# Kernel tuning notes

Measured on AMD Instinct MI355X. Metric: run time of the kernel, lower is better.

## Reference

```python
import jax, jax.numpy as jnp
import numpy as np

KS = 3          # ksize
PAD = 1         # (ksize-1)//2 * dilation, dilation=1

def setup_inputs() -> dict:
    key = jax.random.key(0)
    k1, k2, k3, k4 = jax.random.split(key, 4)
    B, NI, C, H, W = 4, 64, 64, 256, 256
    features = jax.random.normal(k1, (B, NI, H, W), jnp.float32)
    inpt = jax.random.normal(k2, (B, C, H, W), jnp.float32)
    # get_filter: Conv2d(ni, ksize**2, 3, padding=1 reflect, stride=1)
    w = jax.random.normal(k3, (KS * KS, NI, 3, 3), jnp.float32) * 0.05
    b = jax.random.normal(k4, (KS * KS,), jnp.float32) * 0.01
    return {"features": features, "inpt": inpt, "w": w, "b": b}

def reference(features, inpt, w, b):
    # 1) predict per-pixel filters: 3x3 conv with reflect padding
    fpad = jnp.pad(features, ((0, 0), (0, 0), (1, 1), (1, 1)), mode="reflect")
    ff = jax.lax.conv_general_dilated(
        fpad, w, window_strides=(1, 1), padding="VALID",
        dimension_numbers=("NCHW", "OIHW", "NCHW"),
    ) + b[None, :, None, None]                       # [B, 9, H, W]
    ff = jax.nn.softmax(ff, axis=1)                  # softmax over the 9 taps

    # 2) apply per-pixel filter to inpt (shared across channels)
    B, C, H, W = inpt.shape
    ipad = jnp.pad(inpt, ((0, 0), (0, 0), (PAD, PAD), (PAD, PAD)), mode="reflect")
    # unfold: taps in row-major (ki, kj) order, matching torch nn.Unfold
    patches = jnp.stack(
        [ipad[:, :, i:i + H, j:j + W] for i in range(KS) for j in range(KS)],
        axis=2,
    )                                                # [B, C, 9, H, W]
    # out[b,c,h,w] = sum_k patches[b,c,k,h,w] * ff[b,k,h,w]
    return jnp.einsum("bckhw,bkhw->bchw", patches, ff)
```

## Files before the change

kernel.cpp:

```cpp
#include <hip/hip_runtime.h>
#include <math.h>

#define BB 4
#define NI 64
#define CC 64
#define HH 256
#define WW 256
#define HW (HH * WW)

#define TW 64
#define TH 8
#define SR 10
#define SC 66
#define SE 660
#define BUFW 672
#define BUFSTRIDE 1344

__device__ __forceinline__ int refl(int i, int n) {
    i = (i < 0) ? -i : i;
    return (i >= n) ? (2 * n - 2 - i) : i;
}

__global__ __launch_bounds__(512) void pff_lds(
    const float* __restrict__ features,
    const float* __restrict__ inpt,
    const float* __restrict__ wgt,
    const float* __restrict__ bias,
    float* __restrict__ out)
{
    __shared__ float lds[4608];

    const int tid  = threadIdx.x;
    const int half = __builtin_amdgcn_readfirstlane(tid >> 8);
    const int p    = tid & 255;
    const int c    = p & 63;
    const int tr   = p >> 6;
    const int W0   = blockIdx.x * TW;
    const int H0   = blockIdx.y * TH;
    const int b    = blockIdx.z;

    int goff[3], loff[3];
    #pragma unroll
    for (int t = 0; t < 3; ++t) {
        int e = p + 256 * t;
        if (e >= SE) e -= 148;
        loff[t] = e;
        const int row = e / SC;
        const int col = e - row * SC;
        const int gh = refl(H0 - 1 + row, HH);
        const int gw = refl(W0 - 1 + col, WW);
        goff[t] = gh * WW + gw;
    }

    float accA[9], accB[9];
    #pragma unroll
    for (int k = 0; k < 9; ++k) { accA[k] = 0.f; accB[k] = 0.f; }

    const float* fb = features + (size_t)b * NI * HW + (size_t)half * 32 * HW;
    float r0 = fb[goff[0]], r1 = fb[goff[1]], r2 = fb[goff[2]];

    for (int ni = 0; ni < 32; ++ni) {
        float* bw = &lds[(ni & 1) * BUFSTRIDE + half * BUFW];
        bw[loff[0]] = r0; bw[loff[1]] = r1; bw[loff[2]] = r2;
        if (ni < 31) {
            const float* fn = fb + (size_t)(ni + 1) * HW;
            r0 = fn[goff[0]]; r1 = fn[goff[1]]; r2 = fn[goff[2]];
        }
        __syncthreads();

        float f[12];
        #pragma unroll
        for (int rr = 0; rr < 4; ++rr) {
            const float* br = bw + (2 * tr + rr) * SC + c;
            f[rr * 3 + 0] = br[0];
            f[rr * 3 + 1] = br[1];
            f[rr * 3 + 2] = br[2];
        }

        const float* wn = wgt + (half * 32 + ni) * 9;
        #pragma unroll
        for (int k = 0; k < 9; ++k) {
            const float* wk = wn + k * (NI * 9);
            const float w0 = wk[0], w1 = wk[1], w2 = wk[2];
            const float w3 = wk[3], w4 = wk[4], w5 = wk[5];
            const float w6 = wk[6], w7 = wk[7], w8 = wk[8];
            accA[k] = fmaf(f[0],  w0, accA[k]);
            accB[k] = fmaf(f[3],  w0, accB[k]);
            accA[k] = fmaf(f[1],  w1, accA[k]);
            accB[k] = fmaf(f[4],  w1, accB[k]);
            accA[k] = fmaf(f[2],  w2, accA[k]);
            accB[k] = fmaf(f[5],  w2, accB[k]);
            accA[k] = fmaf(f[3],  w3, accA[k]);
            accB[k] = fmaf(f[6],  w3, accB[k]);
            accA[k] = fmaf(f[4],  w4, accA[k]);
            accB[k] = fmaf(f[7],  w4, accB[k]);
            accA[k] = fmaf(f[5],  w5, accA[k]);
            accB[k] = fmaf(f[8],  w5, accB[k]);
            accA[k] = fmaf(f[6],  w6, accA[k]);
            accB[k] = fmaf(f[9],  w6, accB[k]);
            accA[k] = fmaf(f[7],  w7, accA[k]);
            accB[k] = fmaf(f[10], w7, accB[k]);
            accA[k] = fmaf(f[8],  w8, accA[k]);
            accB[k] = fmaf(f[11], w8, accB[k]);
        }
    }

    __syncthreads();
    #pragma unroll
    for (int k = 0; k < 9; ++k) lds[half * 2304 + k * 256 + p] = accA[k];
    __syncthreads();
    #pragma unroll
    for (int k = 0; k < 9; ++k)
        accA[k] = lds[k * 256 + p] + lds[2304 + k * 256 + p] + bias[k];
    __syncthreads();
    #pragma unroll
    for (int k = 0; k < 9; ++k) lds[half * 2304 + k * 256 + p] = accB[k];
    __syncthreads();
    #pragma unroll
    for (int k = 0; k < 9; ++k)
        accB[k] = lds[k * 256 + p] + lds[2304 + k * 256 + p] + bias[k];

    {
        float m = accA[0];
        #pragma unroll
        for (int k = 1; k < 9; ++k) m = fmaxf(m, accA[k]);
        float s = 0.f;
        #pragma unroll
        for (int k = 0; k < 9; ++k) { accA[k] = __expf(accA[k] - m); s += accA[k]; }
        const float inv = 1.f / s;
        #pragma unroll
        for (int k = 0; k < 9; ++k) accA[k] *= inv;
    }
    {
        float m = accB[0];
        #pragma unroll
        for (int k = 1; k < 9; ++k) m = fmaxf(m, accB[k]);
        float s = 0.f;
        #pragma unroll
        for (int k = 0; k < 9; ++k) { accB[k] = __expf(accB[k] - m); s += accB[k]; }
        const float inv = 1.f / s;
        #pragma unroll
        for (int k = 0; k < 9; ++k) accB[k] *= inv;
    }

    const float* ib = inpt + (size_t)b * CC * HW + (size_t)half * 32 * HW;
    float* ob       = out  + (size_t)b * CC * HW + (size_t)half * 32 * HW;
    const int oA = (H0 + 2 * tr) * WW + W0 + c;
    const int oB = oA + WW;

    r0 = ib[goff[0]]; r1 = ib[goff[1]]; r2 = ib[goff[2]];
    __syncthreads();

    for (int ch = 0; ch < 32; ++ch) {
        float* bw = &lds[(ch & 1) * BUFSTRIDE + half * BUFW];
        bw[loff[0]] = r0; bw[loff[1]] = r1; bw[loff[2]] = r2;
        if (ch < 31) {
            const float* in2 = ib + (size_t)(ch + 1) * HW;
            r0 = in2[goff[0]]; r1 = in2[goff[1]]; r2 = in2[goff[2]];
        }
        __syncthreads();

        float f[12];
        #pragma unroll
        for (int rr = 0; rr < 4; ++rr) {
            const float* br = bw + (2 * tr + rr) * SC + c;
            f[rr * 3 + 0] = br[0];
            f[rr * 3 + 1] = br[1];
            f[rr * 3 + 2] = br[2];
        }

        float vA = accA[0] * f[0];
        float vB = accB[0] * f[3];
        vA = fmaf(accA[1], f[1],  vA);  vB = fmaf(accB[1], f[4],  vB);
        vA = fmaf(accA[2], f[2],  vA);  vB = fmaf(accB[2], f[5],  vB);
        vA = fmaf(accA[3], f[3],  vA);  vB = fmaf(accB[3], f[6],  vB);
        vA = fmaf(accA[4], f[4],  vA);  vB = fmaf(accB[4], f[7],  vB);
        vA = fmaf(accA[5], f[5],  vA);  vB = fmaf(accB[5], f[8],  vB);
        vA = fmaf(accA[6], f[6],  vA);  vB = fmaf(accB[6], f[9],  vB);
        vA = fmaf(accA[7], f[7],  vA);  vB = fmaf(accB[7], f[10], vB);
        vA = fmaf(accA[8], f[8],  vA);  vB = fmaf(accB[8], f[11], vB);
        ob[(size_t)ch * HW + oA] = vA;
        ob[(size_t)ch * HW + oB] = vB;
    }
}

extern "C" void kernel_launch(void* const* d_in, const int* in_sizes, int n_in,
                              void* d_out, int out_size, void* d_ws, size_t ws_size,
                              hipStream_t stream) {
    const float* features = (const float*)d_in[0];
    const float* inpt     = (const float*)d_in[1];
    const float* wgt      = (const float*)d_in[2];
    const float* bias     = (const float*)d_in[3];
    float* out            = (float*)d_out;

    dim3 grid(WW / TW, HH / TH, BB);
    dim3 block(512);
    pff_lds<<<grid, block, 0, stream>>>(features, inpt, wgt, bias, out);
}
```

Before: 74.34 us.

## Give each wavefront a private LDS staging tile to drop block barriers

Each of the eight wavefronts now stages its own 4x66 halo tile in a private double-buffered LDS region. This removes the per-iteration __syncthreads in both the conv loop and the apply loop, relying on wave-synchronous execution instead. The cost is redundant global loads of overlapping halo rows, about twice the staged data, and more LDS use. The first inpt slice load is also hoisted above the cross-half reduction so it overlaps with that step.

New measurement: 70.30 us. 5.4% less time.

```diff
diff --git a/kernel.cpp b/kernel.cpp
--- a/kernel.cpp
+++ b/kernel.cpp
@@ -8,70 +8,69 @@
 #define WW 256
 #define HW (HH * WW)
 
-#define TW 64
-#define TH 8
-#define SR 10
-#define SC 66
-#define SE 660
-#define BUFW 672
-#define BUFSTRIDE 1344
+#define SRW 68
+#define BUFW 272
+#define NBUF 2
 
 __device__ __forceinline__ int refl(int i, int n) {
     i = (i < 0) ? -i : i;
     return (i >= n) ? (2 * n - 2 - i) : i;
 }
 
-__global__ __launch_bounds__(512) void pff_lds(
+__global__ __launch_bounds__(512) void pff_wave(
     const float* __restrict__ features,
     const float* __restrict__ inpt,
     const float* __restrict__ wgt,
     const float* __restrict__ bias,
     float* __restrict__ out)
 {
-    __shared__ float lds[4608];
+    __shared__ float stage[8][NBUF * BUFW];
+    __shared__ float part[2][9][256];
 
     const int tid  = threadIdx.x;
-    const int half = __builtin_amdgcn_readfirstlane(tid >> 8);
+    const int wv   = __builtin_amdgcn_readfirstlane(tid >> 6);
+    const int half = wv >> 2;
+    const int tr   = wv & 3;
+    const int l    = tid & 63;
     const int p    = tid & 255;
-    const int c    = p & 63;
-    const int tr   = p >> 6;
-    const int W0   = blockIdx.x * TW;
-    const int H0   = blockIdx.y * TH;
-    const int b    = blockIdx.z;
+    const int W0 = blockIdx.x * 64;
+    const int H0 = blockIdx.y * 8;
+    const int b  = blockIdx.z;
 
-    int goff[3], loff[3];
+    int goff[5], loff[5];
     #pragma unroll
-    for (int t = 0; t < 3; ++t) {
-        int e = p + 256 * t;
-        if (e >= SE) e -= 148;
-        loff[t] = e;
-        const int row = e / SC;
-        const int col = e - row * SC;
-        const int gh = refl(H0 - 1 + row, HH);
-        const int gw = refl(W0 - 1 + col, WW);
-        goff[t] = gh * WW + gw;
+    for (int t = 0; t < 5; ++t) {
+        const int e = (t < 4) ? (l + 64 * t) : (256 + (l & 7));
+        const int row = e / 66, col = e - row * 66;
+        loff[t] = row * SRW + col;
+        goff[t] = refl(H0 + 2 * tr - 1 + row, HH) * WW + refl(W0 - 1 + col, WW);
     }
+    const bool do5 = (l < 8);
 
     float accA[9], accB[9];
     #pragma unroll
     for (int k = 0; k < 9; ++k) { accA[k] = 0.f; accB[k] = 0.f; }
 
+    float* sb = &stage[wv][0];
+
     const float* fb = features + (size_t)b * NI * HW + (size_t)half * 32 * HW;
-    float r0 = fb[goff[0]], r1 = fb[goff[1]], r2 = fb[goff[2]];
+    float r0 = fb[goff[0]], r1 = fb[goff[1]], r2 = fb[goff[2]], r3 = fb[goff[3]];
+    float r4 = do5 ? fb[goff[4]] : 0.f;
 
     for (int ni = 0; ni < 32; ++ni) {
-        float* bw = &lds[(ni & 1) * BUFSTRIDE + half * BUFW];
-        bw[loff[0]] = r0; bw[loff[1]] = r1; bw[loff[2]] = r2;
+        float* bw = sb + (ni & 1) * BUFW;
+        bw[loff[0]] = r0; bw[loff[1]] = r1; bw[loff[2]] = r2; bw[loff[3]] = r3;
+        if (do5) bw[loff[4]] = r4;
         if (ni < 31) {
             const float* fn = fb + (size_t)(ni + 1) * HW;
-            r0 = fn[goff[0]]; r1 = fn[goff[1]]; r2 = fn[goff[2]];
+            r0 = fn[goff[0]]; r1 = fn[goff[1]]; r2 = fn[goff[2]]; r3 = fn[goff[3]];
+            if (do5) r4 = fn[goff[4]];
         }
-        __syncthreads();
 
         float f[12];
         #pragma unroll
         for (int rr = 0; rr < 4; ++rr) {
-            const float* br = bw + (2 * tr + rr) * SC + c;
+            const float* br = bw + rr * SRW + l;
             f[rr * 3 + 0] = br[0];
             f[rr * 3 + 1] = br[1];
             f[rr * 3 + 2] = br[2];
@@ -105,20 +104,21 @@
         }
     }
 
+    const float* ib = inpt + (size_t)b * CC * HW + (size_t)half * 32 * HW;
+    r0 = ib[goff[0]]; r1 = ib[goff[1]]; r2 = ib[goff[2]]; r3 = ib[goff[3]];
+    if (do5) r4 = ib[goff[4]];
+
+    #pragma unroll
+    for (int k = 0; k < 9; ++k) part[half][k][p] = accA[k];
     __syncthreads();
     #pragma unroll
-    for (int k = 0; k < 9; ++k) lds[half * 2304 + k * 256 + p] = accA[k];
+    for (int k = 0; k < 9; ++k) accA[k] = part[0][k][p] + part[1][k][p] + bias[k];
     __syncthreads();
     #pragma unroll
-    for (int k = 0; k < 9; ++k)
-        accA[k] = lds[k * 256 + p] + lds[2304 + k * 256 + p] + bias[k];
+    for (int k = 0; k < 9; ++k) part[half][k][p] = accB[k];
     __syncthreads();
     #pragma unroll
-    for (int k = 0; k < 9; ++k) lds[half * 2304 + k * 256 + p] = accB[k];
-    __syncthreads();
-    #pragma unroll
-    for (int k = 0; k < 9; ++k)
-        accB[k] = lds[k * 256 + p] + lds[2304 + k * 256 + p] + bias[k];
+    for (int k = 0; k < 9; ++k) accB[k] = part[0][k][p] + part[1][k][p] + bias[k];
 
     {
         float m = accA[0];
@@ -143,27 +143,24 @@
         for (int k = 0; k < 9; ++k) accB[k] *= inv;
     }
 
-    const float* ib = inpt + (size_t)b * CC * HW + (size_t)half * 32 * HW;
-    float* ob       = out  + (size_t)b * CC * HW + (size_t)half * 32 * HW;
-    const int oA = (H0 + 2 * tr) * WW + W0 + c;
+    float* ob = out + (size_t)b * CC * HW + (size_t)half * 32 * HW;
+    const int oA = (H0 + 2 * tr) * WW + W0 + l;
     const int oB = oA + WW;
 
-    r0 = ib[goff[0]]; r1 = ib[goff[1]]; r2 = ib[goff[2]];
-    __syncthreads();
-
     for (int ch = 0; ch < 32; ++ch) {
-        float* bw = &lds[(ch & 1) * BUFSTRIDE + half * BUFW];
-        bw[loff[0]] = r0; bw[loff[1]] = r1; bw[loff[2]] = r2;
+        float* bw = sb + (ch & 1) * BUFW;
+        bw[loff[0]] = r0; bw[loff[1]] = r1; bw[loff[2]] = r2; bw[loff[3]] = r3;
+        if (do5) bw[loff[4]] = r4;
         if (ch < 31) {
             const float* in2 = ib + (size_t)(ch + 1) * HW;
-            r0 = in2[goff[0]]; r1 = in2[goff[1]]; r2 = in2[goff[2]];
+            r0 = in2[goff[0]]; r1 = in2[goff[1]]; r2 = in2[goff[2]]; r3 = in2[goff[3]];
+            if (do5) r4 = in2[goff[4]];
         }
-        __syncthreads();
 
         float f[12];
         #pragma unroll
         for (int rr = 0; rr < 4; ++rr) {
-            const float* br = bw + (2 * tr + rr) * SC + c;
+            const float* br = bw + rr * SRW + l;
             f[rr * 3 + 0] = br[0];
             f[rr * 3 + 1] = br[1];
             f[rr * 3 + 2] = br[2];
@@ -193,7 +190,7 @@
     const float* bias     = (const float*)d_in[3];
     float* out            = (float*)d_out;
 
-    dim3 grid(WW / TW, HH / TH, BB);
+    dim3 grid(WW / 64, HH / 8, BB);
     dim3 block(512);
-    pff_lds<<<grid, block, 0, stream>>>(features, inpt, wgt, bias, out);
+    pff_wave<<<grid, block, 0, stream>>>(features, inpt, wgt, bias, out);
 }
```
